# Kernel optimization log

Measured on AMD Instinct MI355X. Metric: run time of the kernel, lower is better.

Reference implementation:

```python
import jax, jax.numpy as jnp
import numpy as np

INPUT_SIZE = 1
HIDDEN_SIZE = 50
OUTPUT_SIZE = 1
BATCH = 16384
SEQ_LEN = 2048


def setup_inputs() -> dict:
    key = jax.random.key(0)
    ks = jax.random.split(key, 8)
    s_ih = 1.0 / np.sqrt(HIDDEN_SIZE)
    x = jax.random.normal(ks[0], (BATCH, SEQ_LEN, INPUT_SIZE), dtype=jnp.float32)
    # PyTorch nn.LSTM params: weight_ih_l0 [4H, I], weight_hh_l0 [4H, H], biases [4H]
    w_ih = jax.random.uniform(ks[1], (4 * HIDDEN_SIZE, INPUT_SIZE), jnp.float32, -s_ih, s_ih)
    w_hh = jax.random.uniform(ks[2], (4 * HIDDEN_SIZE, HIDDEN_SIZE), jnp.float32, -s_ih, s_ih)
    b_ih = jax.random.uniform(ks[3], (4 * HIDDEN_SIZE,), jnp.float32, -s_ih, s_ih)
    b_hh = jax.random.uniform(ks[4], (4 * HIDDEN_SIZE,), jnp.float32, -s_ih, s_ih)
    # fc head: Linear(hidden_size, output_size)
    w_fc = jax.random.uniform(ks[5], (OUTPUT_SIZE, HIDDEN_SIZE), jnp.float32, -s_ih, s_ih)
    b_fc = jax.random.uniform(ks[6], (OUTPUT_SIZE,), jnp.float32, -s_ih, s_ih)
    return {"x": x, "w_ih": w_ih, "w_hh": w_hh, "b_ih": b_ih, "b_hh": b_hh,
            "w_fc": w_fc, "b_fc": b_fc}


def reference(x, w_ih, w_hh, b_ih, b_hh, w_fc, b_fc):
    B = x.shape[0]
    H = w_hh.shape[1]
    xT = jnp.swapaxes(x, 0, 1)                      # [T, B, I]
    # precompute input contribution to gates for all timesteps: [T, B, 4H]
    x_proj = jnp.einsum('tbi,gi->tbg', xT, w_ih) + b_ih + b_hh

    def step(carry, xp):
        h, c = carry
        gates = xp + h @ w_hh.T                     # [B, 4H]
        i, f, g, o = jnp.split(gates, 4, axis=-1)   # PyTorch gate order: i, f, g, o
        i = jax.nn.sigmoid(i)
        f = jax.nn.sigmoid(f)
        g = jnp.tanh(g)
        o = jax.nn.sigmoid(o)
        c = f * c + i * g
        h = o * jnp.tanh(c)
        return (h, c), None

    h0 = jnp.zeros((B, H), x.dtype)
    (h_last, _), _ = jax.lax.scan(step, (h0, h0), x_proj)
    # fc applied to last timestep's hidden state
    return h_last @ w_fc.T + b_fc                   # [B, 1]
```

## Files before the change

kernel.cpp:

```cpp
#include <hip/hip_runtime.h>
#include <cstdint>

typedef __attribute__((ext_vector_type(8))) short short8;
typedef __attribute__((ext_vector_type(4))) float f32x4;
typedef __attribute__((ext_vector_type(2))) float f32x2;

#define TPB  256
#define MB   16
#define HS   50
#define HSTR 72
#define XSTR 68
#define L2E  1.4426950408889634f
#define L2E2 2.8853900817779268f

__device__ __forceinline__ float ex2(float x) {
#if __has_builtin(__builtin_amdgcn_exp2f)
  return __builtin_amdgcn_exp2f(x);
#else
  float r; asm("v_exp_f32 %0, %1" : "=v"(r) : "v"(x)); return r;
#endif
}
__device__ __forceinline__ float rcp_(float x) {
#if __has_builtin(__builtin_amdgcn_rcpf)
  return __builtin_amdgcn_rcpf(x);
#else
  float r; asm("v_rcp_f32 %0, %1" : "=v"(r) : "v"(x)); return r;
#endif
}
__device__ __forceinline__ unsigned short bf16_rne(float f) {
  unsigned r;
  asm("v_cvt_pk_bf16_f32 %0, %1, %2" : "=v"(r) : "v"(f), "v"(f));
  return (unsigned short)r;
}
__device__ __forceinline__ unsigned cvtpk2(float a, float b) {
  unsigned r;
  asm("v_cvt_pk_bf16_f32 %0, %1, %2" : "=v"(r) : "v"(a), "v"(b));
  return r;
}
__device__ __forceinline__ float bf16f(unsigned short h) {
  union { unsigned u; float f; } v; v.u = ((unsigned)h) << 16; return v.f;
}
__device__ __forceinline__ unsigned packx(float f) {
  unsigned short hi = bf16_rne(f);
  unsigned short lo = bf16_rne(f - bf16f(hi));
  return (unsigned)hi | ((unsigned)lo << 16);
}
__device__ __forceinline__ int swcol(int row, int col) {
  return (((col >> 3) ^ ((row >> 2) & 3)) << 3) | (col & 7);
}

__global__ __launch_bounds__(TPB, 4)
void lstm_mfma7(const float* __restrict__ x,
                const float* __restrict__ w_ih,
                const float* __restrict__ w_hh,
                const float* __restrict__ b_ih,
                const float* __restrict__ b_hh,
                const float* __restrict__ w_fc,
                const float* __restrict__ b_fc,
                float* __restrict__ out, int T)
{
  __shared__ __attribute__((aligned(16))) unsigned short hbuf[2][MB][HSTR];
  __shared__ __attribute__((aligned(16))) unsigned x_lds[2][MB][XSTR];

  const int tid  = threadIdx.x;
  const int wid  = tid >> 6;
  const int lane = tid & 63;
  const int l15  = lane & 15;
  const int lhi  = lane >> 4;
  const int b0   = blockIdx.x * MB;
  const int j    = wid * 16 + l15;
  const bool jval = (j < HS);
  const bool inj  = (lhi == 2);

  short8 Wh[4][2];
  #pragma unroll
  for (int s = 0; s < 4; ++s) {
    const float sc = (s == 2) ? L2E2 : L2E;
    float wsc = 0.f, bsc = 0.f;
    if (jval) {
      int row = s * HS + j;
      wsc = w_ih[row] * sc;
      bsc = (b_ih[row] + b_hh[row]) * sc;
    }
    const unsigned short wh = bf16_rne(wsc);
    const unsigned short wl = bf16_rne(wsc - bf16f(wh));
    const unsigned short bh = bf16_rne(bsc);
    const unsigned short bl = bf16_rne(bsc - bf16f(bh));
    #pragma unroll
    for (int i = 0; i < 8; ++i) {
      int k = lhi * 8 + i;
      Wh[s][0][i] = (short)(jval ? bf16_rne(w_hh[(s * HS + j) * HS + k] * sc) : 0);
    }
    #pragma unroll
    for (int i = 0; i < 8; ++i) {
      int k = 32 + lhi * 8 + i;
      unsigned short hv = 0;
      if (jval) {
        if (k < HS)                  hv = bf16_rne(w_hh[(s * HS + j) * HS + k] * sc);
        else if (k == 50 || k == 51) hv = wh;
        else if (k == 52)            hv = wl;
        else if (k == 53)            hv = bh;
        else if (k == 54)            hv = bl;
      }
      Wh[s][1][i] = (short)hv;
    }
  }

  for (int idx = tid; idx < 2 * MB * HSTR; idx += TPB)
    (&hbuf[0][0][0])[idx] = 0;
  {
    int bb = tid >> 4, tt = (tid & 15) * 4;
    const f32x4 v = *(const f32x4*)(x + (size_t)(b0 + bb) * T + tt);
    uint4 up;
    up.x = packx(v[0]); up.y = packx(v[1]); up.z = packx(v[2]); up.w = packx(v[3]);
    *(uint4*)&x_lds[0][bb][tt] = up;
  }
  __syncthreads();

  const int keyr  = (l15 >> 2) & 3;
  const int offA0 = l15 * HSTR + ((lhi ^ keyr) << 3);
  const int offA1 = l15 * HSTR + (((lhi + 4) ^ keyr) << 3);
  const int offW  = l15 * HSTR + ((((wid * 2 + (lhi >> 1)) ^ keyr) << 3)) + (lhi & 1) * 4;

  f32x2 cA = {0.f, 0.f}, cB = {0.f, 0.f};
  f32x4 xf = {0.f, 0.f, 0.f, 0.f};
  const int nch = T >> 6;

  auto STEP = [&](const unsigned short* hr, unsigned short* hw, int t) {
    if ((t & 63) == 16) {
      int c1 = (t >> 6) + 1;
      if (c1 < nch)
        xf = *(const f32x4*)(x + (size_t)(b0 + (tid >> 4)) * T + c1 * 64 + (tid & 15) * 4);
    }
    if ((t & 63) == 44) {
      int c1 = (t >> 6) + 1;
      if (c1 < nch) {
        uint4 up;
        up.x = packx(xf[0]); up.y = packx(xf[1]);
        up.z = packx(xf[2]); up.w = packx(xf[3]);
        *(uint4*)&x_lds[c1 & 1][tid >> 4][(tid & 15) * 4] = up;
      }
    }

    const unsigned xp = x_lds[(t >> 6) & 1][l15][t & 63];
    const short8 B0 = *(const short8*)(hr + offA0);
    union { short8 s8; unsigned u[4]; } b1;
    b1.s8 = *(const short8*)(hr + offA1);
    b1.u[1] = inj ? xp : b1.u[1];
    b1.u[2] = inj ? ((xp & 0xFFFFu) | 0x3F800000u) : b1.u[2];
    b1.u[3] = inj ? 0x00003F80u : b1.u[3];

    __builtin_amdgcn_s_setprio(1);
    f32x4 acc[4];
    #pragma unroll
    for (int s = 0; s < 4; ++s) {
      acc[s] = __builtin_amdgcn_mfma_f32_16x16x32_bf16(Wh[s][0], B0,
                   (f32x4){0.f, 0.f, 0.f, 0.f}, 0, 0, 0);
      acc[s] = __builtin_amdgcn_mfma_f32_16x16x32_bf16(Wh[s][1], b1.s8, acc[s], 0, 0, 0);
    }
    __builtin_amdgcn_s_setprio(0);

    f32x2 h2A, h2B;
    {
      f32x2 u, v, w, z, q, rD, r3, vm1;
      u[0] = ex2(-acc[0][0]); u[1] = ex2(-acc[0][1]);
      v[0] = ex2( acc[2][0]); v[1] = ex2( acc[2][1]);
      w[0] = ex2(-acc[1][0]); w[1] = ex2(-acc[1][1]);
      z[0] = ex2(-acc[3][0]); z[1] = ex2(-acc[3][1]);
      f32x2 t1 = (u + 1.f) * (v + 1.f);
      f32x2 wp = w + 1.f;
      f32x2 D  = t1 * wp;
      rD[0] = rcp_(D[0]); rD[1] = rcp_(D[1]);
      vm1[0] = fmaf(v[0], L2E2, -L2E2);
      vm1[1] = fmaf(v[1], L2E2, -L2E2);
      f32x2 num = cA * t1 + vm1 * wp;
      f32x2 cn = num * rD;
      cn[0] = fminf(fmaxf(cn[0], -86.f), 86.f);
      cn[1] = fminf(fmaxf(cn[1], -86.f), 86.f);
      cA = cn;
      q[0] = ex2(cn[0]); q[1] = ex2(cn[1]);
      f32x2 t3 = (z + 1.f) * (q + 1.f);
      r3[0] = rcp_(t3[0]); r3[1] = rcp_(t3[1]);
      h2A = (q - 1.f) * r3;
    }
    {
      f32x2 u, v, w, z, q, rD, r3, vm1;
      u[0] = ex2(-acc[0][2]); u[1] = ex2(-acc[0][3]);
      v[0] = ex2( acc[2][2]); v[1] = ex2( acc[2][3]);
      w[0] = ex2(-acc[1][2]); w[1] = ex2(-acc[1][3]);
      z[0] = ex2(-acc[3][2]); z[1] = ex2(-acc[3][3]);
      f32x2 t1 = (u + 1.f) * (v + 1.f);
      f32x2 wp = w + 1.f;
      f32x2 D  = t1 * wp;
      rD[0] = rcp_(D[0]); rD[1] = rcp_(D[1]);
      vm1[0] = fmaf(v[0], L2E2, -L2E2);
      vm1[1] = fmaf(v[1], L2E2, -L2E2);
      f32x2 num = cB * t1 + vm1 * wp;
      f32x2 cn = num * rD;
      cn[0] = fminf(fmaxf(cn[0], -86.f), 86.f);
      cn[1] = fminf(fmaxf(cn[1], -86.f), 86.f);
      cB = cn;
      q[0] = ex2(cn[0]); q[1] = ex2(cn[1]);
      f32x2 t3 = (z + 1.f) * (q + 1.f);
      r3[0] = rcp_(t3[0]); r3[1] = rcp_(t3[1]);
      h2B = (q - 1.f) * r3;
    }

    uint2 hwv;
    hwv.x = cvtpk2(h2A[0], h2A[1]);
    hwv.y = cvtpk2(h2B[0], h2B[1]);
    *(uint2*)(hw + offW) = hwv;

    __syncthreads();
  };

  unsigned short* hb0 = &hbuf[0][0][0];
  unsigned short* hb1 = &hbuf[1][0][0];
  for (int tb = 0; tb < T; tb += 2) {
    STEP(hb0, hb1, tb);
    STEP(hb1, hb0, tb + 1);
  }

  if (tid < MB) {
    const unsigned short* hfin = hb0 + tid * HSTR;
    float s = 0.f;
    for (int jj = 0; jj < HS; ++jj)
      s = fmaf(bf16f(hfin[swcol(tid, jj)]), w_fc[jj], s);
    out[b0 + tid] = s + b_fc[0];
  }
}

extern "C" void kernel_launch(void* const* d_in, const int* in_sizes, int n_in,
                              void* d_out, int out_size, void* d_ws, size_t ws_size,
                              hipStream_t stream) {
  const float* x    = (const float*)d_in[0];
  const float* w_ih = (const float*)d_in[1];
  const float* w_hh = (const float*)d_in[2];
  const float* b_ih = (const float*)d_in[3];
  const float* b_hh = (const float*)d_in[4];
  const float* w_fc = (const float*)d_in[5];
  const float* b_fc = (const float*)d_in[6];
  float* out = (float*)d_out;

  const int B = out_size;
  const int T = in_sizes[0] / B;

  dim3 grid(B / MB), block(TPB);
  hipLaunchKernelGGL(lstm_mfma7, grid, block, 0, stream,
                     x, w_ih, w_hh, b_ih, b_hh, w_fc, b_fc, out, T);
}
```

Baseline: 1.963 ms.

## Skip dead hidden units in last wave, rotate wave roles, restructure chunk loop

Waves are assigned hidden-unit groups with a per-block rotation, so the partly empty group (units 48-63, only 48-49 valid) lands on different SIMDs across blocks. That group's wave computes only the first half of its gate nonlinearities and writes a single packed word, skipping the second half whose rows are padding. The time loop is rebuilt as per-chunk inner loops with the x prefetch and LDS pack placed between sub-loops, removing the per-step modulo branches. The aim is to balance transcendental work across SIMDs and trim per-step control overhead. The cost is more code paths and a per-block wave-role rotation that must stay consistent with the hidden-state layout.

```diff
diff --git a/kernel.cpp b/kernel.cpp
--- a/kernel.cpp
+++ b/kernel.cpp
@@ -50,14 +50,14 @@
 }
 
 __global__ __launch_bounds__(TPB, 4)
-void lstm_mfma7(const float* __restrict__ x,
-                const float* __restrict__ w_ih,
-                const float* __restrict__ w_hh,
-                const float* __restrict__ b_ih,
-                const float* __restrict__ b_hh,
-                const float* __restrict__ w_fc,
-                const float* __restrict__ b_fc,
-                float* __restrict__ out, int T)
+void lstm_mfma10(const float* __restrict__ x,
+                 const float* __restrict__ w_ih,
+                 const float* __restrict__ w_hh,
+                 const float* __restrict__ b_ih,
+                 const float* __restrict__ b_hh,
+                 const float* __restrict__ w_fc,
+                 const float* __restrict__ b_fc,
+                 float* __restrict__ out, int T)
 {
   __shared__ __attribute__((aligned(16))) unsigned short hbuf[2][MB][HSTR];
   __shared__ __attribute__((aligned(16))) unsigned x_lds[2][MB][XSTR];
@@ -68,9 +68,12 @@
   const int l15  = lane & 15;
   const int lhi  = lane >> 4;
   const int b0   = blockIdx.x * MB;
-  const int j    = wid * 16 + l15;
-  const bool jval = (j < HS);
-  const bool inj  = (lhi == 2);
+  const int rho  = (blockIdx.x >> 8) & 3;
+  const int g    = (wid + rho) & 3;
+  const int j    = g * 16 + l15;
+  const bool jval  = (j < HS);
+  const bool light = (g == 3);
+  const bool inj   = (lhi == 2);
 
   short8 Wh[4][2];
   #pragma unroll
@@ -120,29 +123,38 @@
   const int keyr  = (l15 >> 2) & 3;
   const int offA0 = l15 * HSTR + ((lhi ^ keyr) << 3);
   const int offA1 = l15 * HSTR + (((lhi + 4) ^ keyr) << 3);
-  const int offW  = l15 * HSTR + ((((wid * 2 + (lhi >> 1)) ^ keyr) << 3)) + (lhi & 1) * 4;
+  const int offW  = l15 * HSTR + ((((g * 2 + (lhi >> 1)) ^ keyr) << 3)) + (lhi & 1) * 4;
 
   f32x2 cA = {0.f, 0.f}, cB = {0.f, 0.f};
   f32x4 xf = {0.f, 0.f, 0.f, 0.f};
   const int nch = T >> 6;
 
-  auto STEP = [&](const unsigned short* hr, unsigned short* hw, int t) {
-    if ((t & 63) == 16) {
-      int c1 = (t >> 6) + 1;
-      if (c1 < nch)
-        xf = *(const f32x4*)(x + (size_t)(b0 + (tid >> 4)) * T + c1 * 64 + (tid & 15) * 4);
-    }
-    if ((t & 63) == 44) {
-      int c1 = (t >> 6) + 1;
-      if (c1 < nch) {
-        uint4 up;
-        up.x = packx(xf[0]); up.y = packx(xf[1]);
-        up.z = packx(xf[2]); up.w = packx(xf[3]);
-        *(uint4*)&x_lds[c1 & 1][tid >> 4][(tid & 15) * 4] = up;
-      }
-    }
-
-    const unsigned xp = x_lds[(t >> 6) & 1][l15][t & 63];
+  auto ELEM = [&](f32x2 ai, f32x2 af, f32x2 ag, f32x2 ao, f32x2& c2) -> f32x2 {
+    f32x2 u, v, w, z, q, rD, r3, vm1;
+    u[0] = ex2(-ai[0]); u[1] = ex2(-ai[1]);
+    v[0] = ex2( ag[0]); v[1] = ex2( ag[1]);
+    w[0] = ex2(-af[0]); w[1] = ex2(-af[1]);
+    z[0] = ex2(-ao[0]); z[1] = ex2(-ao[1]);
+    f32x2 t1 = (u + 1.f) * (v + 1.f);
+    f32x2 wp = w + 1.f;
+    f32x2 D  = t1 * wp;
+    rD[0] = rcp_(D[0]); rD[1] = rcp_(D[1]);
+    vm1[0] = fmaf(v[0], L2E2, -L2E2);
+    vm1[1] = fmaf(v[1], L2E2, -L2E2);
+    f32x2 num = c2 * t1 + vm1 * wp;
+    f32x2 cn = num * rD;
+    cn[0] = fminf(fmaxf(cn[0], -86.f), 86.f);
+    cn[1] = fminf(fmaxf(cn[1], -86.f), 86.f);
+    c2 = cn;
+    q[0] = ex2(cn[0]); q[1] = ex2(cn[1]);
+    f32x2 t3 = (z + 1.f) * (q + 1.f);
+    r3[0] = rcp_(t3[0]); r3[1] = rcp_(t3[1]);
+    return (q - 1.f) * r3;
+  };
+
+  auto STEP = [&](const unsigned short* hr, unsigned short* hw,
+                  const unsigned* xrow, int slot) {
+    const unsigned xp = xrow[slot];
     const short8 B0 = *(const short8*)(hr + offA0);
     union { short8 s8; unsigned u[4]; } b1;
     b1.s8 = *(const short8*)(hr + offA1);
@@ -160,65 +172,50 @@
     }
     __builtin_amdgcn_s_setprio(0);
 
-    f32x2 h2A, h2B;
-    {
-      f32x2 u, v, w, z, q, rD, r3, vm1;
-      u[0] = ex2(-acc[0][0]); u[1] = ex2(-acc[0][1]);
-      v[0] = ex2( acc[2][0]); v[1] = ex2( acc[2][1]);
-      w[0] = ex2(-acc[1][0]); w[1] = ex2(-acc[1][1]);
-      z[0] = ex2(-acc[3][0]); z[1] = ex2(-acc[3][1]);
-      f32x2 t1 = (u + 1.f) * (v + 1.f);
-      f32x2 wp = w + 1.f;
-      f32x2 D  = t1 * wp;
-      rD[0] = rcp_(D[0]); rD[1] = rcp_(D[1]);
-      vm1[0] = fmaf(v[0], L2E2, -L2E2);
-      vm1[1] = fmaf(v[1], L2E2, -L2E2);
-      f32x2 num = cA * t1 + vm1 * wp;
-      f32x2 cn = num * rD;
-      cn[0] = fminf(fmaxf(cn[0], -86.f), 86.f);
-      cn[1] = fminf(fmaxf(cn[1], -86.f), 86.f);
-      cA = cn;
-      q[0] = ex2(cn[0]); q[1] = ex2(cn[1]);
-      f32x2 t3 = (z + 1.f) * (q + 1.f);
-      r3[0] = rcp_(t3[0]); r3[1] = rcp_(t3[1]);
-      h2A = (q - 1.f) * r3;
-    }
-    {
-      f32x2 u, v, w, z, q, rD, r3, vm1;
-      u[0] = ex2(-acc[0][2]); u[1] = ex2(-acc[0][3]);
-      v[0] = ex2( acc[2][2]); v[1] = ex2( acc[2][3]);
-      w[0] = ex2(-acc[1][2]); w[1] = ex2(-acc[1][3]);
-      z[0] = ex2(-acc[3][2]); z[1] = ex2(-acc[3][3]);
-      f32x2 t1 = (u + 1.f) * (v + 1.f);
-      f32x2 wp = w + 1.f;
-      f32x2 D  = t1 * wp;
-      rD[0] = rcp_(D[0]); rD[1] = rcp_(D[1]);
-      vm1[0] = fmaf(v[0], L2E2, -L2E2);
-      vm1[1] = fmaf(v[1], L2E2, -L2E2);
-      f32x2 num = cB * t1 + vm1 * wp;
-      f32x2 cn = num * rD;
-      cn[0] = fminf(fmaxf(cn[0], -86.f), 86.f);
-      cn[1] = fminf(fmaxf(cn[1], -86.f), 86.f);
-      cB = cn;
-      q[0] = ex2(cn[0]); q[1] = ex2(cn[1]);
-      f32x2 t3 = (z + 1.f) * (q + 1.f);
-      r3[0] = rcp_(t3[0]); r3[1] = rcp_(t3[1]);
-      h2B = (q - 1.f) * r3;
-    }
-
-    uint2 hwv;
-    hwv.x = cvtpk2(h2A[0], h2A[1]);
-    hwv.y = cvtpk2(h2B[0], h2B[1]);
-    *(uint2*)(hw + offW) = hwv;
+    f32x2 h2A = ELEM((f32x2){acc[0][0], acc[0][1]}, (f32x2){acc[1][0], acc[1][1]},
+                     (f32x2){acc[2][0], acc[2][1]}, (f32x2){acc[3][0], acc[3][1]}, cA);
+    unsigned hx = cvtpk2(h2A[0], h2A[1]);
+    if (!light) {
+      f32x2 h2B = ELEM((f32x2){acc[0][2], acc[0][3]}, (f32x2){acc[1][2], acc[1][3]},
+                       (f32x2){acc[2][2], acc[2][3]}, (f32x2){acc[3][2], acc[3][3]}, cB);
+      uint2 hwv;
+      hwv.x = hx;
+      hwv.y = cvtpk2(h2B[0], h2B[1]);
+      *(uint2*)(hw + offW) = hwv;
+    } else {
+      *(unsigned*)(hw + offW) = hx;
+    }
 
     __syncthreads();
   };
 
   unsigned short* hb0 = &hbuf[0][0][0];
   unsigned short* hb1 = &hbuf[1][0][0];
-  for (int tb = 0; tb < T; tb += 2) {
-    STEP(hb0, hb1, tb);
-    STEP(hb1, hb0, tb + 1);
+
+  for (int ch = 0; ch < nch; ++ch) {
+    const int par = ch & 1;
+    const unsigned* xrow = &x_lds[par][l15][0];
+    int slot = 0;
+    #pragma unroll 1
+    for (int i = 0; i < 8; ++i) {
+      STEP(hb0, hb1, xrow, slot); STEP(hb1, hb0, xrow, slot + 1); slot += 2;
+    }
+    if (ch + 1 < nch)
+      xf = *(const f32x4*)(x + (size_t)(b0 + (tid >> 4)) * T + (ch + 1) * 64 + (tid & 15) * 4);
+    #pragma unroll 1
+    for (int i = 0; i < 14; ++i) {
+      STEP(hb0, hb1, xrow, slot); STEP(hb1, hb0, xrow, slot + 1); slot += 2;
+    }
+    if (ch + 1 < nch) {
+      uint4 up;
+      up.x = packx(xf[0]); up.y = packx(xf[1]);
+      up.z = packx(xf[2]); up.w = packx(xf[3]);
+      *(uint4*)&x_lds[par ^ 1][tid >> 4][(tid & 15) * 4] = up;
+    }
+    #pragma unroll 1
+    for (int i = 0; i < 10; ++i) {
+      STEP(hb0, hb1, xrow, slot); STEP(hb1, hb0, xrow, slot + 1); slot += 2;
+    }
   }
 
   if (tid < MB) {
@@ -246,6 +243,6 @@
   const int T = in_sizes[0] / B;
 
   dim3 grid(B / MB), block(TPB);
-  hipLaunchKernelGGL(lstm_mfma7, grid, block, 0, stream,
+  hipLaunchKernelGGL(lstm_mfma10, grid, block, 0, stream,
                      x, w_ih, w_hh, b_ih, b_hh, w_fc, b_fc, out, T);
 }
```

Measured after the change: 1.930 ms. Within noise of the previous version (-1.7%).
